# Optimization experiments

Measured on AMD Instinct MI355X. Metric: run time of the kernel, lower is better.

## Reference

```python
import jax, jax.numpy as jnp
import numpy as np

HEADS = 8
DIM_HEAD = 64
DIM = 512
INNER = HEADS * DIM_HEAD  # 512
SCALE = DIM_HEAD ** -0.5


def setup_inputs() -> dict:
    key = jax.random.key(0)
    k1, k2, k3, k4 = jax.random.split(key, 4)
    B, N = 2, 4096
    x = jax.random.normal(k1, (B, N, DIM), dtype=jnp.float32)
    # nn.Linear(dim, inner*3, bias=False): weight [3*inner, dim]; y = x @ W.T
    w_qkv = jax.random.normal(k2, (3 * INNER, DIM), dtype=jnp.float32) * (DIM ** -0.5)
    w_out = jax.random.normal(k3, (DIM, INNER), dtype=jnp.float32) * (INNER ** -0.5)
    b_out = jax.random.normal(k4, (DIM,), dtype=jnp.float32) * 0.01
    return {"x": x, "w_qkv": w_qkv, "w_out": w_out, "b_out": b_out, "H": 64, "W": 64}


def reference(x, w_qkv, w_out, b_out, H, W):
    B, N, _ = x.shape
    qkv = jnp.einsum('bnd,ed->bne', x, w_qkv)  # [B, N, 3*inner]
    q, k, v = jnp.split(qkv, 3, axis=-1)
    def to_heads(t):
        return t.reshape(B, N, HEADS, DIM_HEAD).transpose(0, 2, 1, 3)  # b h n d
    q, k, v = to_heads(q), to_heads(k), to_heads(v)
    dots = jnp.einsum('bhid,bhjd->bhij', q, k) * SCALE
    attn = jax.nn.softmax(dots, axis=-1)  # dropout p=0.0 -> identity
    out = jnp.einsum('bhij,bhjd->bhid', attn, v)
    out = out.transpose(0, 2, 1, 3).reshape(B, N, INNER)
    return jnp.einsum('bne,de->bnd', out, w_out) + b_out
```

## Files before the change

kernel.cpp:

```cpp
#include <hip/hip_runtime.h>
#include <hip/hip_bf16.h>

typedef __hip_bfloat16 bf16;
typedef __attribute__((ext_vector_type(8))) short short8;
typedef __attribute__((ext_vector_type(4))) short shortx4;
typedef __attribute__((ext_vector_type(4))) float floatx4;
typedef __attribute__((ext_vector_type(4))) int intx4;

#define MFMA16(a, b, c) __builtin_amdgcn_mfma_f32_16x16x32_bf16((a), (b), (c), 0, 0, 0)
#define EXP2(x) __builtin_amdgcn_exp2f(x)

__device__ __forceinline__ short f2s(float v) {
    return __builtin_bit_cast(short, __float2bfloat16(v));
}

__device__ __forceinline__ int packhi(float lo, float hi) {
    return (int)__builtin_amdgcn_perm(__builtin_bit_cast(unsigned, hi),
                                      __builtin_bit_cast(unsigned, lo),
                                      0x07060302u);
}

__device__ __forceinline__ short8 cvt8v(float4 f0, float4 f1) {
    short8 r;
    r[0] = f2s(f0.x); r[1] = f2s(f0.y); r[2] = f2s(f0.z); r[3] = f2s(f0.w);
    r[4] = f2s(f1.x); r[5] = f2s(f1.y); r[6] = f2s(f1.z); r[7] = f2s(f1.w);
    return r;
}

__device__ __forceinline__ int swz(int row, int chunk) {
    return row * 64 + ((chunk ^ (row & 7)) << 3);
}

__global__ __launch_bounds__(256) void cvt_inputs(
    const float* __restrict__ x, const float* __restrict__ wq,
    const float* __restrict__ wo, bf16* __restrict__ xb,
    bf16* __restrict__ wqb, bf16* __restrict__ wob)
{
    int idx = blockIdx.x * 256 + threadIdx.x;
    const float* src;
    bf16* dst;
    int off;
    if (idx < 524288)      { src = x;  dst = xb;  off = idx; }
    else if (idx < 622592) { src = wq; dst = wqb; off = idx - 524288; }
    else                   { src = wo; dst = wob; off = idx - 622592; }
    float4 f0 = ((const float4*)src)[off * 2];
    float4 f1 = ((const float4*)src)[off * 2 + 1];
    *(short8*)&((short*)dst)[off * 8] = cvt8v(f0, f1);
}

__global__ __launch_bounds__(256) void qkv_gemm(
    const bf16* __restrict__ xb, const bf16* __restrict__ wqb,
    bf16* __restrict__ q, bf16* __restrict__ k, bf16* __restrict__ vt)
{
    __shared__ short pool[20480];
    short (*As)[128][40] = (short(*)[128][40])pool;
    short (*Bs)[128][40] = (short(*)[128][40])(pool + 10240);
    short (*Qt)[144] = (short(*)[144])pool;
    short (*Vt)[136] = (short(*)[136])pool;
    const int t = threadIdx.x;
    const int bm = blockIdx.x * 128;
    const int be = blockIdx.y * 128;
    const int w = t >> 6, lane = t & 63, lq = lane >> 4, lm = lane & 15;
    const int wr = w >> 1, wc = w & 1;
    const int srow = t >> 1, scol = (t & 1) * 16;
    const float C = 0.18033688011112042f;

    const bf16* xp = &xb[(size_t)(bm + srow) * 512 + scol];
    const bf16* wp = &wqb[(size_t)(be + srow) * 512 + scol];

    intx4 xr[2], wr4[2];
    auto issue = [&](int k0) {
        xr[0] = *(const intx4*)(xp + k0);
        xr[1] = *(const intx4*)(xp + k0 + 8);
        wr4[0] = *(const intx4*)(wp + k0);
        wr4[1] = *(const intx4*)(wp + k0 + 8);
    };
    auto commit = [&](int buf) {
        *(intx4*)&As[buf][srow][scol]     = xr[0];
        *(intx4*)&As[buf][srow][scol + 8] = xr[1];
        *(intx4*)&Bs[buf][srow][scol]     = wr4[0];
        *(intx4*)&Bs[buf][srow][scol + 8] = wr4[1];
    };

    floatx4 acc[4][4];
#pragma unroll
    for (int i = 0; i < 4; ++i)
#pragma unroll
        for (int j = 0; j < 4; ++j) acc[i][j] = {0.f, 0.f, 0.f, 0.f};

    issue(0);
    commit(0);
    __syncthreads();
    int cur = 0;
    for (int k0 = 0; k0 < 512; k0 += 32) {
        const bool more = (k0 + 32) < 512;
        if (more) issue(k0 + 32);
        short8 af[4], bf[4];
#pragma unroll
        for (int mt = 0; mt < 4; ++mt) af[mt] = *(const short8*)&As[cur][wr * 64 + mt * 16 + lm][lq * 8];
#pragma unroll
        for (int nt = 0; nt < 4; ++nt) bf[nt] = *(const short8*)&Bs[cur][wc * 64 + nt * 16 + lm][lq * 8];
#pragma unroll
        for (int mt = 0; mt < 4; ++mt)
#pragma unroll
            for (int nt = 0; nt < 4; ++nt)
                acc[mt][nt] = MFMA16(af[mt], bf[nt], acc[mt][nt]);
        if (more) {
            commit(cur ^ 1);
            __syncthreads();
        }
        cur ^= 1;
    }

    const int which = be >> 9;
    __syncthreads();
    if (which < 2) {
        const float scale = (which == 0) ? C : 1.0f;
#pragma unroll
        for (int nt = 0; nt < 4; ++nt) {
            const int e_loc = wc * 64 + nt * 16 + lm;
#pragma unroll
            for (int mt = 0; mt < 4; ++mt)
#pragma unroll
                for (int r = 0; r < 4; ++r)
                    Qt[wr * 64 + mt * 16 + lq * 4 + r][e_loc] = f2s(acc[mt][nt][r] * scale);
        }
        __syncthreads();
        bf16* dst = (which == 0) ? q : k;
        const int tr = t >> 1, th = t & 1;
        const int grow = bm + tr;
        const int b = grow >> 12, n = grow & 4095;
        const int h = ((be + th * 64) & 511) >> 6;
        bf16* p = dst + ((size_t)(b * 8 + h) * 4096 + n) * 64;
#pragma unroll
        for (int c = 0; c < 8; ++c)
            *(intx4*)&p[c * 8] = *(const intx4*)&Qt[tr][th * 64 + c * 8];
    } else {
#pragma unroll
        for (int nt = 0; nt < 4; ++nt) {
            const int e_loc = wc * 64 + nt * 16 + lm;
#pragma unroll
            for (int mt = 0; mt < 4; ++mt) {
                const int col = wr * 64 + 4 * (mt & 1) + 8 * lq + 32 * (mt >> 1);
                shortx4 v4;
#pragma unroll
                for (int r = 0; r < 4; ++r) v4[r] = f2s(acc[mt][nt][r]);
                *(shortx4*)&Vt[e_loc][col] = v4;
            }
        }
        __syncthreads();
        const int b = bm >> 12, n0 = bm & 4095;
        const int h0 = (be - 1024) >> 6;
        const int row = t >> 1, cb = (t & 1) * 64;
        const int h = h0 + (row >> 6), d = row & 63;
        const size_t gb = ((size_t)(b * 8 + h) * 64 + d) * 4096 + n0 + cb;
#pragma unroll
        for (int c = 0; c < 8; ++c)
            *(intx4*)&vt[gb + c * 8] = *(const intx4*)&Vt[row][cb + c * 8];
    }
}

__global__ __launch_bounds__(256, 1) void flash_attn(
    const bf16* __restrict__ q, const bf16* __restrict__ k,
    const bf16* __restrict__ vt, bf16* __restrict__ out)
{
    __shared__ short Qs[16384];
    __shared__ short Ks[2][4096];
    __shared__ short Vs[2][4096];
    const int t = threadIdx.x;
    const int n = blockIdx.x;
    const int L = (n & 7) * 32 + (n >> 3);
    const int i0 = (L & 15) * 256;
    const int bh = L >> 4;
    const int w = t >> 6, lane = t & 63, lq = lane >> 4, lm = lane & 15;
    const floatx4 zero4 = {0.f, 0.f, 0.f, 0.f};

    const size_t nbase = (size_t)bh * 4096 * 64;
    const size_t vbase = (size_t)bh * 64 * 4096;
    const int r0 = t >> 3, ch = t & 7;

#pragma unroll
    for (int it = 0; it < 8; ++it) {
        int row = it * 32 + r0;
        *(intx4*)&Qs[swz(row, ch)] =
            *(const intx4*)&q[nbase + (size_t)(i0 + row) * 64 + ch * 8];
    }

    intx4 kreg[2], vreg[2];
    auto issue = [&](int j0n) {
        kreg[0] = *(const intx4*)&k[nbase + (size_t)(j0n + r0) * 64 + ch * 8];
        kreg[1] = *(const intx4*)&k[nbase + (size_t)(j0n + 32 + r0) * 64 + ch * 8];
        vreg[0] = *(const intx4*)&vt[vbase + (size_t)r0 * 4096 + j0n + ch * 8];
        vreg[1] = *(const intx4*)&vt[vbase + (size_t)(32 + r0) * 4096 + j0n + ch * 8];
    };
    auto commit = [&](int buf) {
        *(intx4*)&Ks[buf][swz(r0, ch)]      = kreg[0];
        *(intx4*)&Ks[buf][swz(32 + r0, ch)] = kreg[1];
        *(intx4*)&Vs[buf][swz(r0, ch)]      = vreg[0];
        *(intx4*)&Vs[buf][swz(32 + r0, ch)] = vreg[1];
    };

    issue(0);
    commit(0);
    __syncthreads();

    short8 aq0[4], aq1[4];
#pragma unroll
    for (int g = 0; g < 4; ++g) {
        const int qrow = w * 64 + g * 16 + lm;
        aq0[g] = *(const short8*)&Qs[swz(qrow, lq)];
        aq1[g] = *(const short8*)&Qs[swz(qrow, 4 + lq)];
    }

    float l_lane[4] = {0.f, 0.f, 0.f, 0.f};
    floatx4 o_acc[4][4];
#pragma unroll
    for (int g = 0; g < 4; ++g)
#pragma unroll
        for (int dt = 0; dt < 4; ++dt) o_acc[g][dt] = zero4;

    int cur = 0;
    for (int j0 = 0; j0 < 4096; j0 += 64) {
        const bool more = (j0 + 64) < 4096;
        if (more) issue(j0 + 64);

        intx4 pka[4], pkb[4];
#pragma unroll
        for (int jt = 0; jt < 4; ++jt) {
            const int krow = jt * 16 + lm;
            short8 bk0 = *(const short8*)&Ks[cur][swz(krow, lq)];
            short8 bk1 = *(const short8*)&Ks[cur][swz(krow, 4 + lq)];
#pragma unroll
            for (int g = 0; g < 4; ++g) {
                floatx4 s4 = MFMA16(bk0, aq0[g], zero4);
                s4 = MFMA16(bk1, aq1[g], s4);
                float e0 = EXP2(s4[0]);
                float e1 = EXP2(s4[1]);
                float e2 = EXP2(s4[2]);
                float e3 = EXP2(s4[3]);
                l_lane[g] += (e0 + e1) + (e2 + e3);
                int p01 = packhi(e0, e1), p23 = packhi(e2, e3);
                if (jt < 2) { pka[g][jt * 2] = p01; pka[g][jt * 2 + 1] = p23; }
                else        { pkb[g][(jt - 2) * 2] = p01; pkb[g][(jt - 2) * 2 + 1] = p23; }
            }
        }

#pragma unroll
        for (int dt = 0; dt < 4; ++dt) {
            const int vrow = dt * 16 + lm;
            short8 av0 = *(const short8*)&Vs[cur][swz(vrow, lq)];
            short8 av1 = *(const short8*)&Vs[cur][swz(vrow, 4 + lq)];
#pragma unroll
            for (int g = 0; g < 4; ++g) {
                o_acc[g][dt] = MFMA16(av0, __builtin_bit_cast(short8, pka[g]), o_acc[g][dt]);
                o_acc[g][dt] = MFMA16(av1, __builtin_bit_cast(short8, pkb[g]), o_acc[g][dt]);
            }
        }

        if (more) {
            commit(cur ^ 1);
            __syncthreads();
        }
        cur ^= 1;
    }

    const int b = bh >> 3, h = bh & 7;
    short* Os = Qs;
    const int obase = w * 1024;
    const int il = lane >> 2, cc = (lane & 3) * 16;
#pragma unroll
    for (int g = 0; g < 4; ++g) {
        float l = l_lane[g];
        l += __shfl_xor(l, 16);
        l += __shfl_xor(l, 32);
        const float inv_l = 1.0f / l;
#pragma unroll
        for (int dt = 0; dt < 4; ++dt)
#pragma unroll
            for (int r = 0; r < 4; ++r)
                Os[obase + lm * 64 + dt * 16 + lq * 4 + r] = f2s(o_acc[g][dt][r] * inv_l);
        const int i = i0 + w * 64 + g * 16 + il;
        intx4 v0 = *(const intx4*)&Os[obase + il * 64 + cc];
        intx4 v1 = *(const intx4*)&Os[obase + il * 64 + cc + 8];
        *(intx4*)&out[((size_t)b * 4096 + i) * 512 + h * 64 + cc] = v0;
        *(intx4*)&out[((size_t)b * 4096 + i) * 512 + h * 64 + cc + 8] = v1;
    }
}

__global__ __launch_bounds__(256) void out_gemm(
    const bf16* __restrict__ a, const bf16* __restrict__ wob,
    const float* __restrict__ bias, float* __restrict__ y)
{
    __shared__ short As[2][128][40];
    __shared__ short Bs[2][64][40];
    const int t = threadIdx.x;
    const int bm = blockIdx.x * 128;
    const int be = blockIdx.y * 64;
    const int w = t >> 6, lane = t & 63, lq = lane >> 4, lm = lane & 15;
    const int wr = w >> 1, wc = w & 1;
    const int srow = t >> 1, scol = (t & 1) * 16;
    const int brow = t >> 2, bcol = (t & 3) * 8;

    const bf16* ap = &a[(size_t)(bm + srow) * 512 + scol];
    const bf16* wp = &wob[(size_t)(be + brow) * 512 + bcol];

    intx4 ar[2], br;
    auto issue = [&](int k0) {
        ar[0] = *(const intx4*)(ap + k0);
        ar[1] = *(const intx4*)(ap + k0 + 8);
        br    = *(const intx4*)(wp + k0);
    };
    auto commit = [&](int buf) {
        *(intx4*)&As[buf][srow][scol]     = ar[0];
        *(intx4*)&As[buf][srow][scol + 8] = ar[1];
        *(intx4*)&Bs[buf][brow][bcol]     = br;
    };

    floatx4 acc[4][2];
#pragma unroll
    for (int i = 0; i < 4; ++i)
#pragma unroll
        for (int j = 0; j < 2; ++j) acc[i][j] = {0.f, 0.f, 0.f, 0.f};

    issue(0);
    commit(0);
    __syncthreads();
    int cur = 0;
    for (int k0 = 0; k0 < 512; k0 += 32) {
        const bool more = (k0 + 32) < 512;
        if (more) issue(k0 + 32);
        short8 af[4], bf[2];
#pragma unroll
        for (int mt = 0; mt < 4; ++mt) af[mt] = *(const short8*)&As[cur][wr * 64 + mt * 16 + lm][lq * 8];
#pragma unroll
        for (int nt = 0; nt < 2; ++nt) bf[nt] = *(const short8*)&Bs[cur][wc * 32 + nt * 16 + lm][lq * 8];
#pragma unroll
        for (int mt = 0; mt < 4; ++mt)
#pragma unroll
            for (int nt = 0; nt < 2; ++nt)
                acc[mt][nt] = MFMA16(af[mt], bf[nt], acc[mt][nt]);
        if (more) {
            commit(cur ^ 1);
            __syncthreads();
        }
        cur ^= 1;
    }

#pragma unroll
    for (int nt = 0; nt < 2; ++nt) {
        const int gcol = be + wc * 32 + nt * 16 + lm;
        const float bv = bias[gcol];
#pragma unroll
        for (int mt = 0; mt < 4; ++mt) {
#pragma unroll
            for (int r = 0; r < 4; ++r) {
                int grow = bm + wr * 64 + mt * 16 + lq * 4 + r;
                y[(size_t)grow * 512 + gcol] = acc[mt][nt][r] + bv;
            }
        }
    }
}

extern "C" void kernel_launch(void* const* d_in, const int* in_sizes, int n_in,
                              void* d_out, int out_size, void* d_ws, size_t ws_size,
                              hipStream_t stream) {
    const float* x     = (const float*)d_in[0];
    const float* w_qkv = (const float*)d_in[1];
    const float* w_out = (const float*)d_in[2];
    const float* b_out = (const float*)d_in[3];

    const size_t HEAD_ELEMS = (size_t)16 * 4096 * 64;
    bf16* qw  = (bf16*)d_ws;
    bf16* kw  = qw + HEAD_ELEMS;
    bf16* vtw = kw + HEAD_ELEMS;
    bf16* aw  = vtw + HEAD_ELEMS;
    bf16* xb  = aw + HEAD_ELEMS;
    bf16* wqb = xb + (size_t)8192 * 512;
    bf16* wob = wqb + (size_t)1536 * 512;
    float* y  = (float*)d_out;

    cvt_inputs<<<2560, 256, 0, stream>>>(x, w_qkv, w_out, xb, wqb, wob);
    qkv_gemm<<<dim3(64, 12), 256, 0, stream>>>(xb, wqb, qw, kw, vtw);
    flash_attn<<<dim3(256), 256, 0, stream>>>(qw, kw, vtw, aw);
    out_gemm<<<dim3(64, 8), 256, 0, stream>>>(aw, wob, b_out, y);
}
```

Measured before the change: 214.8 us.

## Split flash-attention key tiles across wave pairs and double the grid

Each block now handles 128 query rows instead of 256. The two waves that share a query group each take half of every 64-key tile, and their partial outputs and row sums are reduced through shared memory at the end. The grid doubles to 512 blocks and launch bounds allow two blocks per CU, which is meant to fill all CUs on MI355X (256 blocks would leave many idle) and improve latency hiding. In exchange, K/V staging traffic per query row doubles and there is an extra shared-memory reduction at the end.

```diff
diff --git a/kernel.cpp b/kernel.cpp
--- a/kernel.cpp
+++ b/kernel.cpp
@@ -160,19 +160,22 @@
     }
 }
 
-__global__ __launch_bounds__(256, 1) void flash_attn(
+__global__ __launch_bounds__(256, 2) void flash_attn(
     const bf16* __restrict__ q, const bf16* __restrict__ k,
     const bf16* __restrict__ vt, bf16* __restrict__ out)
 {
-    __shared__ short Qs[16384];
-    __shared__ short Ks[2][4096];
-    __shared__ short Vs[2][4096];
+    __shared__ short pool[24576];
+    short* Qs = pool;
+    short* Ks0 = pool + 8192;
+    short* Vs0 = pool + 16384;
     const int t = threadIdx.x;
     const int n = blockIdx.x;
-    const int L = (n & 7) * 32 + (n >> 3);
-    const int i0 = (L & 15) * 256;
-    const int bh = L >> 4;
+    const int L = (n & 7) * 64 + (n >> 3);
+    const int i0 = (L & 31) * 128;
+    const int bh = L >> 5;
     const int w = t >> 6, lane = t & 63, lq = lane >> 4, lm = lane & 15;
+    const int h = w >> 1;
+    const int par = w & 1;
     const floatx4 zero4 = {0.f, 0.f, 0.f, 0.f};
 
     const size_t nbase = (size_t)bh * 4096 * 64;
@@ -180,7 +183,7 @@
     const int r0 = t >> 3, ch = t & 7;
 
 #pragma unroll
-    for (int it = 0; it < 8; ++it) {
+    for (int it = 0; it < 4; ++it) {
         int row = it * 32 + r0;
         *(intx4*)&Qs[swz(row, ch)] =
             *(const intx4*)&q[nbase + (size_t)(i0 + row) * 64 + ch * 8];
@@ -194,10 +197,12 @@
         vreg[1] = *(const intx4*)&vt[vbase + (size_t)(32 + r0) * 4096 + j0n + ch * 8];
     };
     auto commit = [&](int buf) {
-        *(intx4*)&Ks[buf][swz(r0, ch)]      = kreg[0];
-        *(intx4*)&Ks[buf][swz(32 + r0, ch)] = kreg[1];
-        *(intx4*)&Vs[buf][swz(r0, ch)]      = vreg[0];
-        *(intx4*)&Vs[buf][swz(32 + r0, ch)] = vreg[1];
+        short* Kb = Ks0 + buf * 4096;
+        short* Vb = Vs0 + buf * 4096;
+        *(intx4*)&Kb[swz(r0, ch)]      = kreg[0];
+        *(intx4*)&Kb[swz(32 + r0, ch)] = kreg[1];
+        *(intx4*)&Vb[swz(r0, ch)]      = vreg[0];
+        *(intx4*)&Vb[swz(32 + r0, ch)] = vreg[1];
     };
 
     issue(0);
@@ -207,7 +212,7 @@
     short8 aq0[4], aq1[4];
 #pragma unroll
     for (int g = 0; g < 4; ++g) {
-        const int qrow = w * 64 + g * 16 + lm;
+        const int qrow = h * 64 + g * 16 + lm;
         aq0[g] = *(const short8*)&Qs[swz(qrow, lq)];
         aq1[g] = *(const short8*)&Qs[swz(qrow, 4 + lq)];
     }
@@ -219,17 +224,20 @@
 #pragma unroll
         for (int dt = 0; dt < 4; ++dt) o_acc[g][dt] = zero4;
 
+    const int jtb = par * 2;
     int cur = 0;
     for (int j0 = 0; j0 < 4096; j0 += 64) {
         const bool more = (j0 + 64) < 4096;
         if (more) issue(j0 + 64);
-
-        intx4 pka[4], pkb[4];
-#pragma unroll
-        for (int jt = 0; jt < 4; ++jt) {
-            const int krow = jt * 16 + lm;
-            short8 bk0 = *(const short8*)&Ks[cur][swz(krow, lq)];
-            short8 bk1 = *(const short8*)&Ks[cur][swz(krow, 4 + lq)];
+        const short* Kb = Ks0 + cur * 4096;
+        const short* Vb = Vs0 + cur * 4096;
+
+        intx4 pk[4];
+#pragma unroll
+        for (int q2 = 0; q2 < 2; ++q2) {
+            const int krow = (jtb + q2) * 16 + lm;
+            short8 bk0 = *(const short8*)&Kb[swz(krow, lq)];
+            short8 bk1 = *(const short8*)&Kb[swz(krow, 4 + lq)];
 #pragma unroll
             for (int g = 0; g < 4; ++g) {
                 floatx4 s4 = MFMA16(bk0, aq0[g], zero4);
@@ -239,22 +247,18 @@
                 float e2 = EXP2(s4[2]);
                 float e3 = EXP2(s4[3]);
                 l_lane[g] += (e0 + e1) + (e2 + e3);
-                int p01 = packhi(e0, e1), p23 = packhi(e2, e3);
-                if (jt < 2) { pka[g][jt * 2] = p01; pka[g][jt * 2 + 1] = p23; }
-                else        { pkb[g][(jt - 2) * 2] = p01; pkb[g][(jt - 2) * 2 + 1] = p23; }
+                pk[g][q2 * 2]     = packhi(e0, e1);
+                pk[g][q2 * 2 + 1] = packhi(e2, e3);
             }
         }
 
 #pragma unroll
         for (int dt = 0; dt < 4; ++dt) {
             const int vrow = dt * 16 + lm;
-            short8 av0 = *(const short8*)&Vs[cur][swz(vrow, lq)];
-            short8 av1 = *(const short8*)&Vs[cur][swz(vrow, 4 + lq)];
-#pragma unroll
-            for (int g = 0; g < 4; ++g) {
-                o_acc[g][dt] = MFMA16(av0, __builtin_bit_cast(short8, pka[g]), o_acc[g][dt]);
-                o_acc[g][dt] = MFMA16(av1, __builtin_bit_cast(short8, pkb[g]), o_acc[g][dt]);
-            }
+            short8 av = *(const short8*)&Vb[swz(vrow, par * 4 + lq)];
+#pragma unroll
+            for (int g = 0; g < 4; ++g)
+                o_acc[g][dt] = MFMA16(av, __builtin_bit_cast(short8, pk[g]), o_acc[g][dt]);
         }
 
         if (more) {
@@ -264,26 +268,47 @@
         cur ^= 1;
     }
 
-    const int b = bh >> 3, h = bh & 7;
-    short* Os = Qs;
-    const int obase = w * 1024;
-    const int il = lane >> 2, cc = (lane & 3) * 16;
-#pragma unroll
-    for (int g = 0; g < 4; ++g) {
-        float l = l_lane[g];
-        l += __shfl_xor(l, 16);
-        l += __shfl_xor(l, 32);
-        const float inv_l = 1.0f / l;
-#pragma unroll
-        for (int dt = 0; dt < 4; ++dt)
-#pragma unroll
-            for (int r = 0; r < 4; ++r)
-                Os[obase + lm * 64 + dt * 16 + lq * 4 + r] = f2s(o_acc[g][dt][r] * inv_l);
-        const int i = i0 + w * 64 + g * 16 + il;
-        intx4 v0 = *(const intx4*)&Os[obase + il * 64 + cc];
-        intx4 v1 = *(const intx4*)&Os[obase + il * 64 + cc + 8];
-        *(intx4*)&out[((size_t)b * 4096 + i) * 512 + h * 64 + cc] = v0;
-        *(intx4*)&out[((size_t)b * 4096 + i) * 512 + h * 64 + cc + 8] = v1;
+    __syncthreads();
+    float* Red = (float*)(pool + 8192);
+    float* Lx  = (float*)pool;
+    if (par == 1) {
+#pragma unroll
+        for (int g = 0; g < 4; ++g) {
+            Lx[h * 256 + g * 64 + lane] = l_lane[g];
+#pragma unroll
+            for (int dt = 0; dt < 4; ++dt)
+#pragma unroll
+                for (int r = 0; r < 4; ++r)
+                    Red[h * 4096 + ((g * 4 + dt) * 4 + r) * 64 + lane] = o_acc[g][dt][r];
+        }
+    }
+    __syncthreads();
+    if (par == 0) {
+        const int b = bh >> 3, hd = bh & 7;
+        short* Os = pool + 1024 + h * 1024;
+        const int il = lane >> 2, cc = (lane & 3) * 16;
+#pragma unroll
+        for (int g = 0; g < 4; ++g) {
+            float l = l_lane[g] + Lx[h * 256 + g * 64 + lane];
+#pragma unroll
+            for (int dt = 0; dt < 4; ++dt)
+#pragma unroll
+                for (int r = 0; r < 4; ++r)
+                    o_acc[g][dt][r] += Red[h * 4096 + ((g * 4 + dt) * 4 + r) * 64 + lane];
+            l += __shfl_xor(l, 16);
+            l += __shfl_xor(l, 32);
+            const float inv_l = 1.0f / l;
+#pragma unroll
+            for (int dt = 0; dt < 4; ++dt)
+#pragma unroll
+                for (int r = 0; r < 4; ++r)
+                    Os[lm * 64 + dt * 16 + lq * 4 + r] = f2s(o_acc[g][dt][r] * inv_l);
+            const int i = i0 + h * 64 + g * 16 + il;
+            intx4 v0 = *(const intx4*)&Os[il * 64 + cc];
+            intx4 v1 = *(const intx4*)&Os[il * 64 + cc + 8];
+            *(intx4*)&out[((size_t)b * 4096 + i) * 512 + hd * 64 + cc] = v0;
+            *(intx4*)&out[((size_t)b * 4096 + i) * 512 + hd * 64 + cc + 8] = v1;
+        }
     }
 }
 
@@ -381,6 +406,6 @@
 
     cvt_inputs<<<2560, 256, 0, stream>>>(x, w_qkv, w_out, xb, wqb, wob);
     qkv_gemm<<<dim3(64, 12), 256, 0, stream>>>(xb, wqb, qw, kw, vtw);
-    flash_attn<<<dim3(256), 256, 0, stream>>>(qw, kw, vtw, aw);
+    flash_attn<<<dim3(512), 256, 0, stream>>>(qw, kw, vtw, aw);
     out_gemm<<<dim3(64, 8), 256, 0, stream>>>(aw, wob, b_out, y);
 }
```

Result: faster. 189.3 us (-11.9%).
